# Kernel optimization log

Hardware: AMD Instinct MI355X
Metric: run time of the kernel (lower is better)

The kernel has to match this reference:

```python
import jax, jax.numpy as jnp
import numpy as np

B, D, W = 2048, 512, 512
DEPTH = 6
N_BINS = 2 ** DEPTH          # 64 leaves
N_NODES = 2 ** DEPTH - 1     # 63 inner nodes


def build_indices(depth: int) -> np.ndarray:
    """Root-to-leaf path index table into hstack([probs, 1-probs]).
    Index j selects probs[:, j]; index j + N selects 1 - probs[:, j]."""
    n = 2 ** depth - 1
    paths = []
    for b in range(2 ** depth):
        node, path = 0, []
        for level in range(depth):
            bit = (b >> (depth - 1 - level)) & 1
            path.append(node if bit == 0 else node + n)
            node = 2 * node + 1 + bit
        paths.append(path)
    return np.asarray(paths, dtype=np.int32)  # [2**depth, depth]


def setup_inputs() -> dict:
    key = jax.random.key(0)
    k1, k2, k3, k4 = jax.random.split(key, 4)
    x = jax.random.normal(k1, (B, D), dtype=jnp.float32)
    ray = jax.random.normal(k2, (1, D), dtype=jnp.float32)  # kaiming-normal init
    w_i = jnp.zeros((1, N_NODES), dtype=jnp.float32)
    b_i = jax.random.normal(k3, (1, N_NODES), dtype=jnp.float32)
    a_i = 5.0 * jnp.ones((1, N_NODES), dtype=jnp.float32)
    # kaiming-normal over fan_in = input_width
    inner_transforms = jax.random.normal(k4, (N_BINS, D, W), dtype=jnp.float32) * np.float32((2.0 / D) ** 0.5)
    idx = jnp.asarray(build_indices(DEPTH))  # [64, 6] int32
    return {"x": x, "ray": ray, "w_i": w_i, "b_i": b_i, "a_i": a_i,
            "inner_transforms": inner_transforms, "idx": idx}


def reference(x, ray, w_i, b_i, a_i, inner_transforms, idx):
    eps = 1e-8
    # angles: arccos(cosine_similarity(x, ray)) / pi  -> [B]
    xn = jnp.maximum(jnp.linalg.norm(x, axis=1), eps)
    rn = jnp.maximum(jnp.linalg.norm(ray, axis=1), eps)  # [1]
    cos = (x @ ray[0]) / (xn * rn)
    angles = jnp.arccos(cos) / jnp.pi  # [B]
    # per-node decision probabilities: [B, N_NODES]
    node_fns = (0.5 + jax.nn.sigmoid(w_i)) * angles[:, None] - jax.nn.sigmoid(b_i)
    decisions = jax.nn.sigmoid(node_fns * (1.0 + a_i))
    # tree-indexed gather + product over path -> soft bin distribution [B, N_BINS]
    stacked = jnp.concatenate([decisions, 1.0 - decisions], axis=1)  # [B, 2N]
    bins, depth = idx.shape
    gathered = stacked[:, idx.reshape(-1)].reshape(x.shape[0], bins, depth)
    distribution = jnp.prod(gathered, axis=2)  # [B, L]
    # per-bin linear transforms, weighted by the distribution
    inner = jnp.einsum('bi,liw->blw', x, inner_transforms)  # [B, L, W]
    return jnp.einsum('bl,blo->bo', distribution, inner)  # [B, W]
```

## Files before the change

kernel.cpp:

```cpp
#include <hip/hip_runtime.h>
#include <math.h>

typedef float  f32x4  __attribute__((ext_vector_type(4)));
typedef float  f32x2  __attribute__((ext_vector_type(2)));
typedef short  bf16x8 __attribute__((ext_vector_type(8)));
typedef unsigned short u16x8 __attribute__((ext_vector_type(8)));
typedef unsigned short u16x4 __attribute__((ext_vector_type(4)));

#define B_ROWS 2048
#define D_DIM  512
#define W_DIM  512
#define N_NODES 63
#define N_BINS  64
#define K_TOT   32768
#define NSPLIT  8
#define LPS     (N_BINS / NSPLIT)
#define DEPS    1e-12f

__device__ __forceinline__ unsigned short f2bf(float f) {
    union { float f; unsigned int u; } v; v.f = f;
    unsigned int u = v.u;
    return (unsigned short)((u + 0x7fffu + ((u >> 16) & 1u)) >> 16);
}

__device__ __forceinline__ float sigmoidf_(float z) {
    return 1.0f / (1.0f + expf(-z));
}

__device__ __forceinline__ void load_lds16(const void* g, void* l) {
    __builtin_amdgcn_global_load_lds(
        (const __attribute__((address_space(1))) unsigned int*)g,
        (__attribute__((address_space(3))) unsigned int*)l,
        16, 0, 0);
}

__global__ __launch_bounds__(256) void k_pre(
    const float* __restrict__ x, const float* __restrict__ ray,
    const float* __restrict__ w_i, const float* __restrict__ b_i,
    const float* __restrict__ a_i, const int* __restrict__ idx,
    const float* __restrict__ T,
    float* __restrict__ dist, unsigned short* __restrict__ xb,
    unsigned short* __restrict__ Tt)
{
    __shared__ float tile[64][65];
    const int bid = blockIdx.x;
    const int t   = threadIdx.x;

    if (bid < 4096) {
        const int i0 = (bid & 7) * 64;
        const int w0 = ((bid >> 3) & 7) * 64;
        const int l  = bid >> 6;

        const int w4 = (t & 15) * 4;
        const int ir = t >> 4;
        const float* src = T + ((size_t)(l * 512 + i0)) * 512 + w0;
#pragma unroll
        for (int p = 0; p < 4; ++p) {
            int i = ir + p * 16;
            f32x4 v = *(const f32x4*)(src + (size_t)i * 512 + w4);
            tile[i][w4 + 0] = v.x; tile[i][w4 + 1] = v.y;
            tile[i][w4 + 2] = v.z; tile[i][w4 + 3] = v.w;
        }
        __syncthreads();
#pragma unroll
        for (int rep = 0; rep < 2; ++rep) {
            int id = t + rep * 256;
            int w  = id >> 3;
            int c  = id & 7;
            u16x8 o;
#pragma unroll
            for (int j = 0; j < 8; ++j) o[j] = f2bf(tile[c * 8 + j][w]);
            *(u16x8*)(Tt + (size_t)(w0 + w) * K_TOT + l * 512 + i0 + c * 8) = o;
        }
        return;
    }

    const int pb   = bid - 4096;
    const int wid  = t >> 6;
    const int lane = t & 63;
    const int row  = pb * 4 + wid;
    const float* xr = x + (size_t)row * D_DIM;

    float dotv = 0.f, xx = 0.f, rr = 0.f;
#pragma unroll
    for (int j = 0; j < 2; ++j) {
        f32x4 xv = *(const f32x4*)(xr  + j * 256 + lane * 4);
        f32x4 rv = *(const f32x4*)(ray + j * 256 + lane * 4);
        dotv += xv.x * rv.x + xv.y * rv.y + xv.z * rv.z + xv.w * rv.w;
        xx   += xv.x * xv.x + xv.y * xv.y + xv.z * xv.z + xv.w * xv.w;
        rr   += rv.x * rv.x + rv.y * rv.y + rv.z * rv.z + rv.w * rv.w;
        u16x4 o;
        o[0] = f2bf(xv.x); o[1] = f2bf(xv.y); o[2] = f2bf(xv.z); o[3] = f2bf(xv.w);
        *(u16x4*)(xb + (size_t)row * D_DIM + j * 256 + lane * 4) = o;
    }
#pragma unroll
    for (int off = 1; off < 64; off <<= 1) {
        dotv += __shfl_xor(dotv, off, 64);
        xx   += __shfl_xor(xx,   off, 64);
        rr   += __shfl_xor(rr,   off, 64);
    }
    float xn = fmaxf(sqrtf(xx), 1e-8f);
    float rn = fmaxf(sqrtf(rr), 1e-8f);
    float cosv = dotv / (xn * rn);
    cosv = fminf(1.f, fmaxf(-1.f, cosv));
    float angle = acosf(cosv) * 0.31830988618379067f;

    float dec = 0.f;
    if (lane < N_NODES) {
        float sw = sigmoidf_(w_i[lane]);
        float sb = sigmoidf_(b_i[lane]);
        float nf = (0.5f + sw) * angle - sb;
        dec = sigmoidf_(nf * (1.0f + a_i[lane]));
    }

    float p = 1.f;
#pragma unroll
    for (int v = 0; v < 6; ++v) {
        int j = idx[lane * 6 + v];
        int node = (j < N_NODES) ? j : j - N_NODES;
        float d = __shfl(dec, node, 64);
        p *= (j < N_NODES) ? d : (1.0f - d);
    }
    dist[(size_t)row * N_BINS + lane] = p;
}

__global__ __launch_bounds__(512, 2) void k_gemm10(
    const unsigned short* __restrict__ xb, const unsigned short* __restrict__ Tt,
    const float* __restrict__ dist, float* __restrict__ part)
{
    __shared__ unsigned short As[3][256 * 64];
    __shared__ unsigned short Bs[3][128 * 64];

    const int b    = blockIdx.x;
    const int z    = b & 7;
    const int tile = b >> 3;
    const int bm0  = (tile & 7) * 256;
    const int bn0  = (tile >> 3) * 128;
    const int l0   = z * LPS;

    const int t    = threadIdx.x;
    const int lane = t & 63;
    const int wid  = t >> 6;
    const int wm = wid >> 1, wn = wid & 1;
    const int lq = lane >> 4, lr = lane & 15;

    const int srow = t >> 3;
    const int c    = t & 7;

    f32x4 acc[4][4];
#pragma unroll
    for (int a = 0; a < 4; ++a)
#pragma unroll
        for (int bb = 0; bb < 4; ++bb)
            acc[a][bb] = (f32x4){0.f, 0.f, 0.f, 0.f};

#define STAGE_A(u_, slot_, g_)                                                \
    {                                                                         \
        const int i0_  = ((u_) & 7) * 64;                                     \
        const int row_ = srow + (g_) * 64;                                    \
        const int cg_  = c ^ (row_ & 7);                                      \
        load_lds16(xb + (size_t)(bm0 + row_) * D_DIM + i0_ + cg_ * 8,         \
                   &As[slot_][row_ * 64 + c * 8]);                            \
    }
#define STAGE_B(u_, slot_, g_)                                                \
    {                                                                         \
        const int l_   = l0 + ((u_) >> 3);                                    \
        const int i0_  = ((u_) & 7) * 64;                                     \
        const int row_ = srow + (g_) * 64;                                    \
        const int cg_  = c ^ (row_ & 7);                                      \
        load_lds16(Tt + (size_t)(bn0 + row_) * K_TOT + (size_t)l_ * 512       \
                       + i0_ + cg_ * 8,                                       \
                   &Bs[slot_][row_ * 64 + c * 8]);                            \
    }

    STAGE_A(0, 0, 0) STAGE_A(0, 0, 1) STAGE_A(0, 0, 2) STAGE_A(0, 0, 3)
    STAGE_B(0, 0, 0) STAGE_B(0, 0, 1)
    STAGE_A(1, 1, 0) STAGE_A(1, 1, 1) STAGE_A(1, 1, 2) STAGE_A(1, 1, 3)
    STAGE_B(1, 1, 0) STAGE_B(1, 1, 1)

    int rs = 0;
    for (int u = 0; u < 64; ++u) {
        if (u < 63) asm volatile("s_waitcnt vmcnt(6)" ::: "memory");
        else        asm volatile("s_waitcnt vmcnt(0)" ::: "memory");
        __builtin_amdgcn_s_barrier();

        if ((u & 7) == 0 && u > 0) {
            const int l = l0 + (u >> 3);
#pragma unroll
            for (int fm = 0; fm < 4; ++fm)
#pragma unroll
                for (int r = 0; r < 4; ++r) {
                    int m = bm0 + wm * 64 + fm * 16 + lq * 4 + r;
                    f32x2 dd = *(const f32x2*)(dist + (size_t)m * N_BINS + (l - 1));
                    float dp = fmaxf(dd.x, DEPS);
                    float dn = fmaxf(dd.y, DEPS);
                    float ratio = dp * __builtin_amdgcn_rcpf(dn);
#pragma unroll
                    for (int fn = 0; fn < 4; ++fn)
                        acc[fm][fn][r] *= ratio;
                }
        }

        const int ws_ = (rs == 0) ? 2 : rs - 1;
        const bool pf = (u + 2 < 64);

        {
            bf16x8 af[4], bfv[4];
#pragma unroll
            for (int fm = 0; fm < 4; ++fm) {
                int m = wm * 64 + fm * 16 + lr;
                af[fm] = *(const bf16x8*)&As[rs][m * 64 + ((lq ^ (m & 7)) * 8)];
            }
#pragma unroll
            for (int fn = 0; fn < 4; ++fn) {
                int n = wn * 64 + fn * 16 + lr;
                bfv[fn] = *(const bf16x8*)&Bs[rs][n * 64 + ((lq ^ (n & 7)) * 8)];
            }
            if (pf) { STAGE_A(u + 2, ws_, 0) STAGE_A(u + 2, ws_, 1) STAGE_A(u + 2, ws_, 2) }
            __builtin_amdgcn_s_setprio(1);
#pragma unroll
            for (int fm = 0; fm < 4; ++fm)
#pragma unroll
                for (int fn = 0; fn < 4; ++fn)
                    acc[fm][fn] = __builtin_amdgcn_mfma_f32_16x16x32_bf16(
                        af[fm], bfv[fn], acc[fm][fn], 0, 0, 0);
            __builtin_amdgcn_s_setprio(0);
        }
        __builtin_amdgcn_s_barrier();
        {
            bf16x8 af[4], bfv[4];
#pragma unroll
            for (int fm = 0; fm < 4; ++fm) {
                int m = wm * 64 + fm * 16 + lr;
                af[fm] = *(const bf16x8*)&As[rs][m * 64 + (((4 + lq) ^ (m & 7)) * 8)];
            }
#pragma unroll
            for (int fn = 0; fn < 4; ++fn) {
                int n = wn * 64 + fn * 16 + lr;
                bfv[fn] = *(const bf16x8*)&Bs[rs][n * 64 + (((4 + lq) ^ (n & 7)) * 8)];
            }
            if (pf) { STAGE_A(u + 2, ws_, 3) STAGE_B(u + 2, ws_, 0) STAGE_B(u + 2, ws_, 1) }
            __builtin_amdgcn_s_setprio(1);
#pragma unroll
            for (int fm = 0; fm < 4; ++fm)
#pragma unroll
                for (int fn = 0; fn < 4; ++fn)
                    acc[fm][fn] = __builtin_amdgcn_mfma_f32_16x16x32_bf16(
                        af[fm], bfv[fn], acc[fm][fn], 0, 0, 0);
            __builtin_amdgcn_s_setprio(0);
        }

        rs = (rs == 2) ? 0 : rs + 1;
    }
#undef STAGE_A
#undef STAGE_B

    float* Cp = part + (size_t)z * (B_ROWS * W_DIM);
#pragma unroll
    for (int fm = 0; fm < 4; ++fm)
#pragma unroll
        for (int r = 0; r < 4; ++r) {
            int m = bm0 + wm * 64 + fm * 16 + lq * 4 + r;
            float dl = fmaxf(dist[(size_t)m * N_BINS + (l0 + LPS - 1)], DEPS);
#pragma unroll
            for (int fn = 0; fn < 4; ++fn) {
                int col = bn0 + wn * 64 + fn * 16 + lr;
                Cp[(size_t)m * W_DIM + col] = acc[fm][fn][r] * dl;
            }
        }
}

__global__ __launch_bounds__(256) void k_reduce(
    const float* __restrict__ part, float* __restrict__ out, int nsplit)
{
    int i = (blockIdx.x * 256 + threadIdx.x) * 4;
    f32x4 s = *(const f32x4*)(part + i);
    for (int p = 1; p < nsplit; ++p)
        s += *(const f32x4*)(part + (size_t)p * (B_ROWS * W_DIM) + i);
    *(f32x4*)(out + i) = s;
}

__global__ __launch_bounds__(256, 2) void k_gemm_bt(
    const float* __restrict__ x, const float* __restrict__ dist,
    const unsigned short* __restrict__ Tt, float* __restrict__ part,
    int kchunk)
{
    __shared__ unsigned short As[128][72];
    __shared__ unsigned short Bs[128][64];

    const int bm0 = blockIdx.x * 128;
    const int bn0 = blockIdx.y * 128;
    const int kbase = blockIdx.z * kchunk;

    const int lane = threadIdx.x & 63;
    const int wid  = threadIdx.x >> 6;
    const int wm = wid >> 1, wn = wid & 1;
    const int lq = lane >> 4, lr = lane & 15;

    f32x4 acc[4][4];
#pragma unroll
    for (int a = 0; a < 4; ++a)
#pragma unroll
        for (int b = 0; b < 4; ++b)
            acc[a][b] = (f32x4){0.f, 0.f, 0.f, 0.f};

    const int iters = kchunk / 64;
    for (int it = 0; it < iters; ++it) {
        const int k0 = kbase + it * 64;
        const int l  = k0 >> 9;
        const int i0 = k0 & 511;
#pragma unroll
        for (int r2 = 0; r2 < 8; ++r2) {
            int id = threadIdx.x + r2 * 256;
            int m  = id >> 4;
            int kc = id & 15;
            float sc = dist[(size_t)(bm0 + m) * N_BINS + l];
            f32x4 v = *(const f32x4*)(x + (size_t)(bm0 + m) * D_DIM + i0 + kc * 4);
            v *= sc;
            unsigned int p0 = (unsigned int)f2bf(v.x) | ((unsigned int)f2bf(v.y) << 16);
            unsigned int p1 = (unsigned int)f2bf(v.z) | ((unsigned int)f2bf(v.w) << 16);
            unsigned int* dp = (unsigned int*)&As[m][kc * 4];
            dp[0] = p0; dp[1] = p1;
        }
#pragma unroll
        for (int r2 = 0; r2 < 4; ++r2) {
            int id = threadIdx.x + r2 * 256;
            int n  = id >> 3;
            int cc = id & 7;
            int cg = cc ^ (n & 7);
            const u16x8 v = *(const u16x8*)(Tt + (size_t)(bn0 + n) * K_TOT + k0 + cg * 8);
            *(u16x8*)&Bs[n][cc * 8] = v;
        }
        __syncthreads();
#pragma unroll
        for (int ks = 0; ks < 2; ++ks) {
            bf16x8 af[4], bfr[4];
#pragma unroll
            for (int fm = 0; fm < 4; ++fm)
                af[fm] = *(const bf16x8*)&As[wm * 64 + fm * 16 + lr][ks * 32 + lq * 8];
#pragma unroll
            for (int fn = 0; fn < 4; ++fn) {
                int nl = wn * 64 + fn * 16 + lr;
                int cs = (ks * 4 + lq) ^ (nl & 7);
                bfr[fn] = *(const bf16x8*)&Bs[nl][cs * 8];
            }
#pragma unroll
            for (int fm = 0; fm < 4; ++fm)
#pragma unroll
                for (int fn = 0; fn < 4; ++fn)
                    acc[fm][fn] = __builtin_amdgcn_mfma_f32_16x16x32_bf16(
                        af[fm], bfr[fn], acc[fm][fn], 0, 0, 0);
        }
        __syncthreads();
    }

    float* Cp = part + (size_t)blockIdx.z * (B_ROWS * W_DIM);
#pragma unroll
    for (int fm = 0; fm < 4; ++fm)
#pragma unroll
        for (int fn = 0; fn < 4; ++fn)
#pragma unroll
            for (int r = 0; r < 4; ++r) {
                int row = bm0 + wm * 64 + fm * 16 + lq * 4 + r;
                int col = bn0 + wn * 64 + fn * 16 + lr;
                Cp[(size_t)row * W_DIM + col] = acc[fm][fn][r];
            }
}

extern "C" void kernel_launch(void* const* d_in, const int* in_sizes, int n_in,
                              void* d_out, int out_size, void* d_ws, size_t ws_size,
                              hipStream_t stream) {
    const float* x   = (const float*)d_in[0];
    const float* ray = (const float*)d_in[1];
    const float* w_i = (const float*)d_in[2];
    const float* b_i = (const float*)d_in[3];
    const float* a_i = (const float*)d_in[4];
    const float* T   = (const float*)d_in[5];
    const int*   idx = (const int*)d_in[6];
    float* out = (float*)d_out;

    char* ws = (char*)d_ws;
    const size_t distBytes = (size_t)B_ROWS * N_BINS * 4;
    const size_t xbBytes   = (size_t)B_ROWS * D_DIM * 2;
    const size_t ttBytes   = (size_t)W_DIM * K_TOT * 2;
    const size_t partBytes = (size_t)B_ROWS * W_DIM * 4;

    float*          dist = (float*)ws;
    unsigned short* xb   = (unsigned short*)(ws + distBytes);
    unsigned short* Tt   = (unsigned short*)(ws + distBytes + xbBytes);

    if (ws_size >= distBytes + xbBytes + ttBytes + (size_t)NSPLIT * partBytes) {
        float* part = (float*)(ws + distBytes + xbBytes + ttBytes);

        k_pre<<<4096 + 512, 256, 0, stream>>>(x, ray, w_i, b_i, a_i, idx, T,
                                              dist, xb, Tt);
        k_gemm10<<<256, 512, 0, stream>>>(xb, Tt, dist, part);
        k_reduce<<<(B_ROWS * W_DIM) / (256 * 4), 256, 0, stream>>>(part, out, NSPLIT);
    } else if (ws_size >= distBytes + xbBytes + ttBytes) {
        k_pre<<<4096 + 512, 256, 0, stream>>>(x, ray, w_i, b_i, a_i, idx, T,
                                              dist, xb, Tt);
        k_gemm_bt<<<dim3(16, 4, 1), 256, 0, stream>>>(x, dist, Tt, out, K_TOT);
    }
}
```

Baseline: 187.5 us.

## Use 4-wave blocks with 128x64 warp tiles and separate partial/sum accumulators

New measurement: 217.6 us. 16.1% more time.

```diff
diff --git a/kernel.cpp b/kernel.cpp
--- a/kernel.cpp
+++ b/kernel.cpp
@@ -124,7 +124,7 @@
     dist[(size_t)row * N_BINS + lane] = p;
 }
 
-__global__ __launch_bounds__(512, 2) void k_gemm10(
+__global__ __launch_bounds__(256, 1) void k_gemm11(
     const unsigned short* __restrict__ xb, const unsigned short* __restrict__ Tt,
     const float* __restrict__ dist, float* __restrict__ part)
 {
@@ -147,17 +147,19 @@
     const int srow = t >> 3;
     const int c    = t & 7;
 
-    f32x4 acc[4][4];
-#pragma unroll
-    for (int a = 0; a < 4; ++a)
-#pragma unroll
-        for (int bb = 0; bb < 4; ++bb)
-            acc[a][bb] = (f32x4){0.f, 0.f, 0.f, 0.f};
+    f32x4 accS[8][4], accP[8][4];
+#pragma unroll
+    for (int a = 0; a < 8; ++a)
+#pragma unroll
+        for (int bb = 0; bb < 4; ++bb) {
+            accS[a][bb] = (f32x4){0.f, 0.f, 0.f, 0.f};
+            accP[a][bb] = (f32x4){0.f, 0.f, 0.f, 0.f};
+        }
 
 #define STAGE_A(u_, slot_, g_)                                                \
     {                                                                         \
         const int i0_  = ((u_) & 7) * 64;                                     \
-        const int row_ = srow + (g_) * 64;                                    \
+        const int row_ = srow + (g_) * 32;                                    \
         const int cg_  = c ^ (row_ & 7);                                      \
         load_lds16(xb + (size_t)(bm0 + row_) * D_DIM + i0_ + cg_ * 8,         \
                    &As[slot_][row_ * 64 + c * 8]);                            \
@@ -166,7 +168,7 @@
     {                                                                         \
         const int l_   = l0 + ((u_) >> 3);                                    \
         const int i0_  = ((u_) & 7) * 64;                                     \
-        const int row_ = srow + (g_) * 64;                                    \
+        const int row_ = srow + (g_) * 32;                                    \
         const int cg_  = c ^ (row_ & 7);                                      \
         load_lds16(Tt + (size_t)(bn0 + row_) * K_TOT + (size_t)l_ * 512       \
                        + i0_ + cg_ * 8,                                       \
@@ -174,41 +176,26 @@
     }
 
     STAGE_A(0, 0, 0) STAGE_A(0, 0, 1) STAGE_A(0, 0, 2) STAGE_A(0, 0, 3)
-    STAGE_B(0, 0, 0) STAGE_B(0, 0, 1)
+    STAGE_A(0, 0, 4) STAGE_A(0, 0, 5) STAGE_A(0, 0, 6) STAGE_A(0, 0, 7)
+    STAGE_B(0, 0, 0) STAGE_B(0, 0, 1) STAGE_B(0, 0, 2) STAGE_B(0, 0, 3)
     STAGE_A(1, 1, 0) STAGE_A(1, 1, 1) STAGE_A(1, 1, 2) STAGE_A(1, 1, 3)
-    STAGE_B(1, 1, 0) STAGE_B(1, 1, 1)
+    STAGE_A(1, 1, 4) STAGE_A(1, 1, 5) STAGE_A(1, 1, 6) STAGE_A(1, 1, 7)
+    STAGE_B(1, 1, 0) STAGE_B(1, 1, 1) STAGE_B(1, 1, 2) STAGE_B(1, 1, 3)
 
     int rs = 0;
     for (int u = 0; u < 64; ++u) {
-        if (u < 63) asm volatile("s_waitcnt vmcnt(6)" ::: "memory");
+        if (u < 63) asm volatile("s_waitcnt vmcnt(12)" ::: "memory");
         else        asm volatile("s_waitcnt vmcnt(0)" ::: "memory");
         __builtin_amdgcn_s_barrier();
 
-        if ((u & 7) == 0 && u > 0) {
-            const int l = l0 + (u >> 3);
-#pragma unroll
-            for (int fm = 0; fm < 4; ++fm)
-#pragma unroll
-                for (int r = 0; r < 4; ++r) {
-                    int m = bm0 + wm * 64 + fm * 16 + lq * 4 + r;
-                    f32x2 dd = *(const f32x2*)(dist + (size_t)m * N_BINS + (l - 1));
-                    float dp = fmaxf(dd.x, DEPS);
-                    float dn = fmaxf(dd.y, DEPS);
-                    float ratio = dp * __builtin_amdgcn_rcpf(dn);
-#pragma unroll
-                    for (int fn = 0; fn < 4; ++fn)
-                        acc[fm][fn][r] *= ratio;
-                }
-        }
-
         const int ws_ = (rs == 0) ? 2 : rs - 1;
         const bool pf = (u + 2 < 64);
 
         {
-            bf16x8 af[4], bfv[4];
-#pragma unroll
-            for (int fm = 0; fm < 4; ++fm) {
-                int m = wm * 64 + fm * 16 + lr;
+            bf16x8 af[8], bfv[4];
+#pragma unroll
+            for (int fm = 0; fm < 8; ++fm) {
+                int m = wm * 128 + fm * 16 + lr;
                 af[fm] = *(const bf16x8*)&As[rs][m * 64 + ((lq ^ (m & 7)) * 8)];
             }
 #pragma unroll
@@ -216,22 +203,41 @@
                 int n = wn * 64 + fn * 16 + lr;
                 bfv[fn] = *(const bf16x8*)&Bs[rs][n * 64 + ((lq ^ (n & 7)) * 8)];
             }
-            if (pf) { STAGE_A(u + 2, ws_, 0) STAGE_A(u + 2, ws_, 1) STAGE_A(u + 2, ws_, 2) }
+            if (pf) {
+                STAGE_A(u + 2, ws_, 0) STAGE_A(u + 2, ws_, 1)
+                STAGE_A(u + 2, ws_, 2) STAGE_A(u + 2, ws_, 3)
+                STAGE_A(u + 2, ws_, 4) STAGE_A(u + 2, ws_, 5)
+                STAGE_A(u + 2, ws_, 6) STAGE_A(u + 2, ws_, 7)
+            }
+            if ((u & 7) == 0 && u > 0) {
+                const int lp = l0 + (u >> 3) - 1;
+#pragma unroll
+                for (int fm = 0; fm < 8; ++fm)
+#pragma unroll
+                    for (int r = 0; r < 4; ++r) {
+                        int m = bm0 + wm * 128 + fm * 16 + lq * 4 + r;
+                        float dv = dist[(size_t)m * N_BINS + lp];
+#pragma unroll
+                        for (int fn = 0; fn < 4; ++fn) {
+                            accS[fm][fn][r] += dv * accP[fm][fn][r];
+                            accP[fm][fn][r] = 0.f;
+                        }
+                    }
+            }
             __builtin_amdgcn_s_setprio(1);
 #pragma unroll
-            for (int fm = 0; fm < 4; ++fm)
+            for (int fm = 0; fm < 8; ++fm)
 #pragma unroll
                 for (int fn = 0; fn < 4; ++fn)
-                    acc[fm][fn] = __builtin_amdgcn_mfma_f32_16x16x32_bf16(
-                        af[fm], bfv[fn], acc[fm][fn], 0, 0, 0);
+                    accP[fm][fn] = __builtin_amdgcn_mfma_f32_16x16x32_bf16(
+                        af[fm], bfv[fn], accP[fm][fn], 0, 0, 0);
             __builtin_amdgcn_s_setprio(0);
         }
-        __builtin_amdgcn_s_barrier();
         {
-            bf16x8 af[4], bfv[4];
-#pragma unroll
-            for (int fm = 0; fm < 4; ++fm) {
-                int m = wm * 64 + fm * 16 + lr;
+            bf16x8 af[8], bfv[4];
+#pragma unroll
+            for (int fm = 0; fm < 8; ++fm) {
+                int m = wm * 128 + fm * 16 + lr;
                 af[fm] = *(const bf16x8*)&As[rs][m * 64 + (((4 + lq) ^ (m & 7)) * 8)];
             }
 #pragma unroll
@@ -239,14 +245,17 @@
                 int n = wn * 64 + fn * 16 + lr;
                 bfv[fn] = *(const bf16x8*)&Bs[rs][n * 64 + (((4 + lq) ^ (n & 7)) * 8)];
             }
-            if (pf) { STAGE_A(u + 2, ws_, 3) STAGE_B(u + 2, ws_, 0) STAGE_B(u + 2, ws_, 1) }
+            if (pf) {
+                STAGE_B(u + 2, ws_, 0) STAGE_B(u + 2, ws_, 1)
+                STAGE_B(u + 2, ws_, 2) STAGE_B(u + 2, ws_, 3)
+            }
             __builtin_amdgcn_s_setprio(1);
 #pragma unroll
-            for (int fm = 0; fm < 4; ++fm)
+            for (int fm = 0; fm < 8; ++fm)
 #pragma unroll
                 for (int fn = 0; fn < 4; ++fn)
-                    acc[fm][fn] = __builtin_amdgcn_mfma_f32_16x16x32_bf16(
-                        af[fm], bfv[fn], acc[fm][fn], 0, 0, 0);
+                    accP[fm][fn] = __builtin_amdgcn_mfma_f32_16x16x32_bf16(
+                        af[fm], bfv[fn], accP[fm][fn], 0, 0, 0);
             __builtin_amdgcn_s_setprio(0);
         }
 
@@ -255,17 +264,19 @@
 #undef STAGE_A
 #undef STAGE_B
 
+    const int ll = l0 + LPS - 1;
     float* Cp = part + (size_t)z * (B_ROWS * W_DIM);
 #pragma unroll
-    for (int fm = 0; fm < 4; ++fm)
+    for (int fm = 0; fm < 8; ++fm)
 #pragma unroll
         for (int r = 0; r < 4; ++r) {
-            int m = bm0 + wm * 64 + fm * 16 + lq * 4 + r;
-            float dl = fmaxf(dist[(size_t)m * N_BINS + (l0 + LPS - 1)], DEPS);
+            int m = bm0 + wm * 128 + fm * 16 + lq * 4 + r;
+            float dv = dist[(size_t)m * N_BINS + ll];
 #pragma unroll
             for (int fn = 0; fn < 4; ++fn) {
                 int col = bn0 + wn * 64 + fn * 16 + lr;
-                Cp[(size_t)m * W_DIM + col] = acc[fm][fn][r] * dl;
+                Cp[(size_t)m * W_DIM + col] =
+                    accS[fm][fn][r] + dv * accP[fm][fn][r];
             }
         }
 }
@@ -394,7 +405,7 @@
 
         k_pre<<<4096 + 512, 256, 0, stream>>>(x, ray, w_i, b_i, a_i, idx, T,
                                               dist, xb, Tt);
-        k_gemm10<<<256, 512, 0, stream>>>(xb, Tt, dist, part);
+        k_gemm11<<<256, 256, 0, stream>>>(xb, Tt, dist, part);
         k_reduce<<<(B_ROWS * W_DIM) / (256 * 4), 256, 0, stream>>>(part, out, NSPLIT);
     } else if (ws_size >= distBytes + xbBytes + ttBytes) {
         k_pre<<<4096 + 512, 256, 0, stream>>>(x, ray, w_i, b_i, a_i, idx, T,
```

## Split K across wave halves with larger per-wave tiles and LDS reduction

Applied to the files above, without the earlier changes.

After: 192.7 us. 1.03x slower.

```diff
diff --git a/kernel.cpp b/kernel.cpp
--- a/kernel.cpp
+++ b/kernel.cpp
@@ -124,12 +124,13 @@
     dist[(size_t)row * N_BINS + lane] = p;
 }
 
-__global__ __launch_bounds__(512, 2) void k_gemm10(
+__global__ __launch_bounds__(512, 2) void k_gemm12(
     const unsigned short* __restrict__ xb, const unsigned short* __restrict__ Tt,
     const float* __restrict__ dist, float* __restrict__ part)
 {
     __shared__ unsigned short As[3][256 * 64];
     __shared__ unsigned short Bs[3][128 * 64];
+    __shared__ float distS[256 * 8];
 
     const int b    = blockIdx.x;
     const int z    = b & 7;
@@ -141,15 +142,17 @@
     const int t    = threadIdx.x;
     const int lane = t & 63;
     const int wid  = t >> 6;
-    const int wm = wid >> 1, wn = wid & 1;
+    const int kh   = wid >> 2;
+    const int pm   = (wid >> 1) & 1;
+    const int pn   = wid & 1;
     const int lq = lane >> 4, lr = lane & 15;
 
     const int srow = t >> 3;
     const int c    = t & 7;
 
-    f32x4 acc[4][4];
-#pragma unroll
-    for (int a = 0; a < 4; ++a)
+    f32x4 acc[8][4];
+#pragma unroll
+    for (int a = 0; a < 8; ++a)
 #pragma unroll
         for (int bb = 0; bb < 4; ++bb)
             acc[a][bb] = (f32x4){0.f, 0.f, 0.f, 0.f};
@@ -173,10 +176,17 @@
                    &Bs[slot_][row_ * 64 + c * 8]);                            \
     }
 
+    {
+        const int dr = t >> 1, dh = t & 1;
+        load_lds16(dist + (size_t)(bm0 + dr) * N_BINS + l0 + dh * 4,
+                   &distS[dr * 8 + dh * 4]);
+    }
     STAGE_A(0, 0, 0) STAGE_A(0, 0, 1) STAGE_A(0, 0, 2) STAGE_A(0, 0, 3)
     STAGE_B(0, 0, 0) STAGE_B(0, 0, 1)
     STAGE_A(1, 1, 0) STAGE_A(1, 1, 1) STAGE_A(1, 1, 2) STAGE_A(1, 1, 3)
     STAGE_B(1, 1, 0) STAGE_B(1, 1, 1)
+
+    const int ko = kh * 4;
 
     int rs = 0;
     for (int u = 0; u < 64; ++u) {
@@ -185,15 +195,16 @@
         __builtin_amdgcn_s_barrier();
 
         if ((u & 7) == 0 && u > 0) {
-            const int l = l0 + (u >> 3);
-#pragma unroll
-            for (int fm = 0; fm < 4; ++fm)
+            const int li = (u >> 3) - 1;
+#pragma unroll
+            for (int fm = 0; fm < 8; ++fm)
 #pragma unroll
                 for (int r = 0; r < 4; ++r) {
-                    int m = bm0 + wm * 64 + fm * 16 + lq * 4 + r;
-                    f32x2 dd = *(const f32x2*)(dist + (size_t)m * N_BINS + (l - 1));
-                    float dp = fmaxf(dd.x, DEPS);
-                    float dn = fmaxf(dd.y, DEPS);
+                    int ml = pm * 128 + fm * 16 + lq * 4 + r;
+                    float d0 = distS[ml * 8 + li];
+                    float d1 = distS[ml * 8 + li + 1];
+                    float dp = fmaxf(d0, DEPS);
+                    float dn = fmaxf(d1, DEPS);
                     float ratio = dp * __builtin_amdgcn_rcpf(dn);
 #pragma unroll
                     for (int fn = 0; fn < 4; ++fn)
@@ -204,70 +215,86 @@
         const int ws_ = (rs == 0) ? 2 : rs - 1;
         const bool pf = (u + 2 < 64);
 
-        {
-            bf16x8 af[4], bfv[4];
-#pragma unroll
-            for (int fm = 0; fm < 4; ++fm) {
-                int m = wm * 64 + fm * 16 + lr;
-                af[fm] = *(const bf16x8*)&As[rs][m * 64 + ((lq ^ (m & 7)) * 8)];
-            }
-#pragma unroll
-            for (int fn = 0; fn < 4; ++fn) {
-                int n = wn * 64 + fn * 16 + lr;
-                bfv[fn] = *(const bf16x8*)&Bs[rs][n * 64 + ((lq ^ (n & 7)) * 8)];
-            }
-            if (pf) { STAGE_A(u + 2, ws_, 0) STAGE_A(u + 2, ws_, 1) STAGE_A(u + 2, ws_, 2) }
-            __builtin_amdgcn_s_setprio(1);
-#pragma unroll
-            for (int fm = 0; fm < 4; ++fm)
-#pragma unroll
-                for (int fn = 0; fn < 4; ++fn)
-                    acc[fm][fn] = __builtin_amdgcn_mfma_f32_16x16x32_bf16(
-                        af[fm], bfv[fn], acc[fm][fn], 0, 0, 0);
-            __builtin_amdgcn_s_setprio(0);
-        }
+        bf16x8 af[8], bfv[4];
+#pragma unroll
+        for (int fm = 0; fm < 8; ++fm) {
+            int m = pm * 128 + fm * 16 + lr;
+            af[fm] = *(const bf16x8*)&As[rs][m * 64 + (((ko + lq) ^ (m & 7)) * 8)];
+        }
+#pragma unroll
+        for (int fn = 0; fn < 2; ++fn) {
+            int n = pn * 64 + fn * 16 + lr;
+            bfv[fn] = *(const bf16x8*)&Bs[rs][n * 64 + (((ko + lq) ^ (n & 7)) * 8)];
+        }
+        if (pf) { STAGE_A(u + 2, ws_, 0) STAGE_A(u + 2, ws_, 1) STAGE_A(u + 2, ws_, 2) }
         __builtin_amdgcn_s_barrier();
-        {
-            bf16x8 af[4], bfv[4];
-#pragma unroll
-            for (int fm = 0; fm < 4; ++fm) {
-                int m = wm * 64 + fm * 16 + lr;
-                af[fm] = *(const bf16x8*)&As[rs][m * 64 + (((4 + lq) ^ (m & 7)) * 8)];
-            }
-#pragma unroll
-            for (int fn = 0; fn < 4; ++fn) {
-                int n = wn * 64 + fn * 16 + lr;
-                bfv[fn] = *(const bf16x8*)&Bs[rs][n * 64 + (((4 + lq) ^ (n & 7)) * 8)];
-            }
-            if (pf) { STAGE_A(u + 2, ws_, 3) STAGE_B(u + 2, ws_, 0) STAGE_B(u + 2, ws_, 1) }
-            __builtin_amdgcn_s_setprio(1);
-#pragma unroll
-            for (int fm = 0; fm < 4; ++fm)
-#pragma unroll
-                for (int fn = 0; fn < 4; ++fn)
-                    acc[fm][fn] = __builtin_amdgcn_mfma_f32_16x16x32_bf16(
-                        af[fm], bfv[fn], acc[fm][fn], 0, 0, 0);
-            __builtin_amdgcn_s_setprio(0);
-        }
+        asm volatile("s_waitcnt lgkmcnt(0)" ::: "memory");
+        __builtin_amdgcn_sched_barrier(0);
+        __builtin_amdgcn_s_setprio(1);
+#pragma unroll
+        for (int fm = 0; fm < 8; ++fm)
+#pragma unroll
+            for (int fn = 0; fn < 2; ++fn)
+                acc[fm][fn] = __builtin_amdgcn_mfma_f32_16x16x32_bf16(
+                    af[fm], bfv[fn], acc[fm][fn], 0, 0, 0);
+        __builtin_amdgcn_s_setprio(0);
+        __builtin_amdgcn_s_barrier();
+
+#pragma unroll
+        for (int fn = 2; fn < 4; ++fn) {
+            int n = pn * 64 + fn * 16 + lr;
+            bfv[fn] = *(const bf16x8*)&Bs[rs][n * 64 + (((ko + lq) ^ (n & 7)) * 8)];
+        }
+        if (pf) { STAGE_A(u + 2, ws_, 3) STAGE_B(u + 2, ws_, 0) STAGE_B(u + 2, ws_, 1) }
+        __builtin_amdgcn_s_barrier();
+        asm volatile("s_waitcnt lgkmcnt(0)" ::: "memory");
+        __builtin_amdgcn_sched_barrier(0);
+        __builtin_amdgcn_s_setprio(1);
+#pragma unroll
+        for (int fm = 0; fm < 8; ++fm)
+#pragma unroll
+            for (int fn = 2; fn < 4; ++fn)
+                acc[fm][fn] = __builtin_amdgcn_mfma_f32_16x16x32_bf16(
+                    af[fm], bfv[fn], acc[fm][fn], 0, 0, 0);
+        __builtin_amdgcn_s_setprio(0);
 
         rs = (rs == 2) ? 0 : rs + 1;
     }
 #undef STAGE_A
 #undef STAGE_B
 
-    float* Cp = part + (size_t)z * (B_ROWS * W_DIM);
-#pragma unroll
-    for (int fm = 0; fm < 4; ++fm)
-#pragma unroll
-        for (int r = 0; r < 4; ++r) {
-            int m = bm0 + wm * 64 + fm * 16 + lq * 4 + r;
-            float dl = fmaxf(dist[(size_t)m * N_BINS + (l0 + LPS - 1)], DEPS);
-#pragma unroll
-            for (int fn = 0; fn < 4; ++fn) {
-                int col = bn0 + wn * 64 + fn * 16 + lr;
-                Cp[(size_t)m * W_DIM + col] = acc[fm][fn][r] * dl;
+    __syncthreads();
+
+    const int pairid = pm * 2 + pn;
+    float* dump = (pairid < 3) ? ((float*)&As[0][0] + pairid * 8192)
+                               : (float*)&Bs[0][0];
+
+    if (kh == 1) {
+#pragma unroll
+        for (int fm = 0; fm < 8; ++fm)
+#pragma unroll
+            for (int fn = 0; fn < 4; ++fn)
+                *(f32x4*)&dump[((fm * 4 + fn) * 64 + lane) * 4] = acc[fm][fn];
+    }
+    __syncthreads();
+    if (kh == 0) {
+        float* Cp = part + (size_t)z * (B_ROWS * W_DIM);
+#pragma unroll
+        for (int fm = 0; fm < 8; ++fm)
+#pragma unroll
+            for (int r = 0; r < 4; ++r) {
+                int ml = pm * 128 + fm * 16 + lq * 4 + r;
+                int m  = bm0 + ml;
+                float dv = distS[ml * 8 + 7];
+#pragma unroll
+                for (int fn = 0; fn < 4; ++fn) {
+                    f32x4 other = *(const f32x4*)&dump[((fm * 4 + fn) * 64 + lane) * 4];
+                    int col = bn0 + pn * 64 + fn * 16 + lr;
+                    Cp[(size_t)m * W_DIM + col] =
+                        (acc[fm][fn][r] + other[r]) * dv;
+                }
             }
-        }
+    }
 }
 
 __global__ __launch_bounds__(256) void k_reduce(
@@ -394,7 +421,7 @@
 
         k_pre<<<4096 + 512, 256, 0, stream>>>(x, ray, w_i, b_i, a_i, idx, T,
                                               dist, xb, Tt);
-        k_gemm10<<<256, 512, 0, stream>>>(xb, Tt, dist, part);
+        k_gemm12<<<256, 512, 0, stream>>>(xb, Tt, dist, part);
         k_reduce<<<(B_ROWS * W_DIM) / (256 * 4), 256, 0, stream>>>(part, out, NSPLIT);
     } else if (ws_size >= distBytes + xbBytes + ttBytes) {
         k_pre<<<4096 + 512, 256, 0, stream>>>(x, ray, w_i, b_i, a_i, idx, T,
```

## Add 256x256-tile GEMM with 16-way bin split and staged double buffering

Applied to the files above, without the earlier changes.

Result: no change. 189.8 us (+1.3%).

```diff
diff --git a/kernel.cpp b/kernel.cpp
--- a/kernel.cpp
+++ b/kernel.cpp
@@ -13,9 +13,10 @@
 #define N_NODES 63
 #define N_BINS  64
 #define K_TOT   32768
-#define NSPLIT  8
-#define LPS     (N_BINS / NSPLIT)
 #define DEPS    1e-12f
+
+#define STR2(x) #x
+#define WAITVM(n) asm volatile("s_waitcnt vmcnt(" STR2(n) ")" ::: "memory")
 
 __device__ __forceinline__ unsigned short f2bf(float f) {
     union { float f; unsigned int u; } v; v.f = f;
@@ -124,6 +125,176 @@
     dist[(size_t)row * N_BINS + lane] = p;
 }
 
+__global__ __launch_bounds__(512, 2) void k_gemm16(
+    const unsigned short* __restrict__ xb, const unsigned short* __restrict__ Tt,
+    const float* __restrict__ dist, float* __restrict__ part)
+{
+    __shared__ unsigned short As[2][256 * 64];
+    __shared__ unsigned short Bs[2][256 * 64];
+    __shared__ float distS[256 * 4];
+
+    const int b    = blockIdx.x;
+    const int xcd  = b & 7;
+    const int g    = b >> 3;
+    const int z    = xcd * 2 + (g & 1);
+    const int tile = g >> 1;
+    const int bm0  = (tile & 7) * 256;
+    const int bn0  = (tile >> 3) * 256;
+    const int l0   = z * 4;
+
+    const int t    = threadIdx.x;
+    const int lane = t & 63;
+    const int wid  = t >> 6;
+    const int wm   = wid >> 2;
+    const int wn   = wid & 3;
+    const int lq = lane >> 4, lr = lane & 15;
+
+    const int srow = t >> 3;
+    const int c    = t & 7;
+
+    f32x4 acc[8][4];
+#pragma unroll
+    for (int a = 0; a < 8; ++a)
+#pragma unroll
+        for (int bb = 0; bb < 4; ++bb)
+            acc[a][bb] = (f32x4){0.f, 0.f, 0.f, 0.f};
+
+#define SGA(u_, slot_, g_)                                                    \
+    {                                                                         \
+        const int i0_  = ((u_) & 7) * 64;                                     \
+        const int row_ = srow + (g_) * 64;                                    \
+        const int cg_  = c ^ (row_ & 7);                                      \
+        load_lds16(xb + (size_t)(bm0 + row_) * D_DIM + i0_ + cg_ * 8,         \
+                   &As[slot_][row_ * 64 + c * 8]);                            \
+    }
+#define SGB(u_, slot_, g_)                                                    \
+    {                                                                         \
+        const int l_   = l0 + ((u_) >> 3);                                    \
+        const int i0_  = ((u_) & 7) * 64;                                     \
+        const int row_ = srow + (g_) * 64;                                    \
+        const int cg_  = c ^ (row_ & 7);                                      \
+        load_lds16(Tt + (size_t)(bn0 + row_) * K_TOT + (size_t)l_ * 512       \
+                       + i0_ + cg_ * 8,                                       \
+                   &Bs[slot_][row_ * 64 + c * 8]);                            \
+    }
+
+#define RD_A(dst, fmb)                                                        \
+    _Pragma("unroll") for (int f = 0; f < 4; ++f)                             \
+    _Pragma("unroll") for (int ks = 0; ks < 2; ++ks) {                        \
+        int row = ((fmb) + f) * 32 + wm * 16 + lr;                            \
+        dst[f][ks] = *(const bf16x8*)&As[rs][row * 64 +                       \
+                       (((ks * 4 + lq) ^ (row & 7)) * 8)];                    \
+    }
+#define RD_B(dst, fnb)                                                        \
+    _Pragma("unroll") for (int f = 0; f < 2; ++f)                             \
+    _Pragma("unroll") for (int ks = 0; ks < 2; ++ks) {                        \
+        int row = ((fnb) + f) * 64 + wn * 16 + lr;                            \
+        dst[f][ks] = *(const bf16x8*)&Bs[rs][row * 64 +                       \
+                       (((ks * 4 + lq) ^ (row & 7)) * 8)];                    \
+    }
+#define MM(fmb, afv, bfv, fnb)                                                \
+    __builtin_amdgcn_s_setprio(1);                                            \
+    _Pragma("unroll") for (int f = 0; f < 4; ++f)                             \
+    _Pragma("unroll") for (int e = 0; e < 2; ++e)                             \
+    _Pragma("unroll") for (int ks = 0; ks < 2; ++ks)                          \
+        acc[(fmb) + f][(fnb) + e] = __builtin_amdgcn_mfma_f32_16x16x32_bf16(  \
+            afv[f][ks], bfv[e][ks], acc[(fmb) + f][(fnb) + e], 0, 0, 0);      \
+    __builtin_amdgcn_s_setprio(0);
+
+#define LGKM0                                                                 \
+    asm volatile("s_waitcnt lgkmcnt(0)" ::: "memory");                        \
+    __builtin_amdgcn_sched_barrier(0);
+
+#define TILE(u_, V0_, V1_, PF_)                                               \
+  {                                                                           \
+    const int rs = (u_) & 1, ss = rs ^ 1;                                     \
+                                                       \
+    RD_A(afr, 0) RD_B(bfr0, 0)                                                \
+    if (PF_) { SGA((u_) + 1, ss, 0) SGA((u_) + 1, ss, 1) }                    \
+    __builtin_amdgcn_s_barrier();                                             \
+    LGKM0                                                                     \
+    MM(0, afr, bfr0, 0)                                                       \
+    WAITVM(V0_);                                                              \
+    __builtin_amdgcn_s_barrier();                                             \
+                                                       \
+    RD_B(bfr1, 2)                                                             \
+    if (PF_) { SGB((u_) + 1, ss, 0) SGB((u_) + 1, ss, 1) }                    \
+    __builtin_amdgcn_s_barrier();                                             \
+    LGKM0                                                                     \
+    MM(0, afr, bfr1, 2)                                                       \
+    WAITVM(V1_);                                                              \
+    __builtin_amdgcn_s_barrier();                                             \
+                                                       \
+    RD_A(afr, 4)                                                              \
+    if (PF_) { SGB((u_) + 1, ss, 2) SGB((u_) + 1, ss, 3) }                    \
+    __builtin_amdgcn_s_barrier();                                             \
+    LGKM0                                                                     \
+    MM(4, afr, bfr0, 0)                                                       \
+    __builtin_amdgcn_s_barrier();                                             \
+                                                       \
+    if (PF_) { SGA((u_) + 1, ss, 2) SGA((u_) + 1, ss, 3) }                    \
+    __builtin_amdgcn_s_barrier();                                             \
+    __builtin_amdgcn_sched_barrier(0);                                        \
+    MM(4, afr, bfr1, 2)                                                       \
+    WAITVM(4);                                                                \
+    __builtin_amdgcn_s_barrier();                                             \
+  }
+
+    bf16x8 afr[4][2], bfr0[2][2], bfr1[2][2];
+
+    if (t < 256)
+        load_lds16(dist + (size_t)(bm0 + t) * N_BINS + l0, &distS[t * 4]);
+    SGA(0, 0, 0) SGA(0, 0, 1)
+    SGB(0, 0, 0) SGB(0, 0, 1)
+    SGB(0, 0, 2) SGB(0, 0, 3)
+    SGA(0, 0, 2) SGA(0, 0, 3)
+    WAITVM(4);
+    __builtin_amdgcn_s_barrier();
+
+    for (int u = 0; u < 31; ++u) {
+        if ((u & 7) == 0 && u > 0) {
+            const int li = (u >> 3) - 1;
+#pragma unroll
+            for (int fm = 0; fm < 8; ++fm)
+#pragma unroll
+                for (int r = 0; r < 4; ++r) {
+                    int ml = fm * 32 + wm * 16 + lq * 4 + r;
+                    float dp = fmaxf(distS[ml * 4 + li],     DEPS);
+                    float dn = fmaxf(distS[ml * 4 + li + 1], DEPS);
+                    float ratio = dp * __builtin_amdgcn_rcpf(dn);
+#pragma unroll
+                    for (int fn = 0; fn < 4; ++fn)
+                        acc[fm][fn][r] *= ratio;
+                }
+        }
+        TILE(u, 4, 4, true)
+    }
+    TILE(31, 2, 0, false)
+
+#undef TILE
+#undef LGKM0
+#undef MM
+#undef RD_A
+#undef RD_B
+#undef SGA
+#undef SGB
+
+    float* Cp = part + (size_t)z * (B_ROWS * W_DIM);
+#pragma unroll
+    for (int fm = 0; fm < 8; ++fm)
+#pragma unroll
+        for (int r = 0; r < 4; ++r) {
+            int ml = fm * 32 + wm * 16 + lq * 4 + r;
+            float dv = fmaxf(distS[ml * 4 + 3], DEPS);
+            int m = bm0 + ml;
+#pragma unroll
+            for (int fn = 0; fn < 4; ++fn) {
+                int col = bn0 + fn * 64 + wn * 16 + lr;
+                Cp[(size_t)m * W_DIM + col] = acc[fm][fn][r] * dv;
+            }
+        }
+}
+
 __global__ __launch_bounds__(512, 2) void k_gemm10(
     const unsigned short* __restrict__ xb, const unsigned short* __restrict__ Tt,
     const float* __restrict__ dist, float* __restrict__ part)
@@ -136,7 +307,7 @@
     const int tile = b >> 3;
     const int bm0  = (tile & 7) * 256;
     const int bn0  = (tile >> 3) * 128;
-    const int l0   = z * LPS;
+    const int l0   = z * 8;
 
     const int t    = threadIdx.x;
     const int lane = t & 63;
@@ -180,8 +351,8 @@
 
     int rs = 0;
     for (int u = 0; u < 64; ++u) {
-        if (u < 63) asm volatile("s_waitcnt vmcnt(6)" ::: "memory");
-        else        asm volatile("s_waitcnt vmcnt(0)" ::: "memory");
+        if (u < 63) WAITVM(6);
+        else        WAITVM(0);
         __builtin_amdgcn_s_barrier();
 
         if ((u & 7) == 0 && u > 0) {
@@ -261,7 +432,7 @@
 #pragma unroll
         for (int r = 0; r < 4; ++r) {
             int m = bm0 + wm * 64 + fm * 16 + lq * 4 + r;
-            float dl = fmaxf(dist[(size_t)m * N_BINS + (l0 + LPS - 1)], DEPS);
+            float dl = fmaxf(dist[(size_t)m * N_BINS + (l0 + 7)], DEPS);
 #pragma unroll
             for (int fn = 0; fn < 4; ++fn) {
                 int col = bn0 + wn * 64 + fn * 16 + lr;
@@ -388,15 +559,23 @@
     float*          dist = (float*)ws;
     unsigned short* xb   = (unsigned short*)(ws + distBytes);
     unsigned short* Tt   = (unsigned short*)(ws + distBytes + xbBytes);
-
-    if (ws_size >= distBytes + xbBytes + ttBytes + (size_t)NSPLIT * partBytes) {
-        float* part = (float*)(ws + distBytes + xbBytes + ttBytes);
-
+    float*          part = (float*)(ws + distBytes + xbBytes + ttBytes);
+
+    const size_t base   = distBytes + xbBytes + ttBytes;
+    const size_t need16 = base + 16 * partBytes;
+    const size_t need8  = base + 8 * partBytes;
+
+    if (ws_size >= need16) {
+        k_pre<<<4096 + 512, 256, 0, stream>>>(x, ray, w_i, b_i, a_i, idx, T,
+                                              dist, xb, Tt);
+        k_gemm16<<<256, 512, 0, stream>>>(xb, Tt, dist, part);
+        k_reduce<<<(B_ROWS * W_DIM) / (256 * 4), 256, 0, stream>>>(part, out, 16);
+    } else if (ws_size >= need8) {
         k_pre<<<4096 + 512, 256, 0, stream>>>(x, ray, w_i, b_i, a_i, idx, T,
                                               dist, xb, Tt);
         k_gemm10<<<256, 512, 0, stream>>>(xb, Tt, dist, part);
-        k_reduce<<<(B_ROWS * W_DIM) / (256 * 4), 256, 0, stream>>>(part, out, NSPLIT);
-    } else if (ws_size >= distBytes + xbBytes + ttBytes) {
+        k_reduce<<<(B_ROWS * W_DIM) / (256 * 4), 256, 0, stream>>>(part, out, 8);
+    } else if (ws_size >= base) {
         k_pre<<<4096 + 512, 256, 0, stream>>>(x, ray, w_i, b_i, a_i, idx, T,
                                               dist, xb, Tt);
         k_gemm_bt<<<dim3(16, 4, 1), 256, 0, stream>>>(x, dist, Tt, out, K_TOT);
```
